# Performance work log

Measured on AMD Instinct MI355X. Metric: run time of the kernel, lower is better.

Reference implementation:

```python
import jax, jax.numpy as jnp
import numpy as np

B, T, D = 64, 32, 256
NFC = 2 * D          # num_inputs_fc = 512
DIMS = [4 * D, NFC, NFC // 2, NFC // 4, NFC // 8, 4]  # last layer padded to 4 outs
H = 4                # camera, rot, trans, plane heads stacked


def setup_inputs() -> dict:
    key = jax.random.key(0)
    ks = jax.random.split(key, 12)
    inp = {
        "emb": jax.random.normal(ks[0], (B, T, D), dtype=jnp.float32),
        # each of n0, n1 in [1,16] so n0+n1 <= T=32 and no divide-by-zero
        "num_planes": jax.random.randint(ks[1], (B, 2), 1, 17, dtype=jnp.int32),
    }
    for i in range(5):
        fan_in = DIMS[i]
        scale = 1.0 / np.sqrt(fan_in)
        inp[f"w{i}"] = jax.random.uniform(ks[2 + 2 * i], (H, DIMS[i], DIMS[i + 1]),
                                           minval=-scale, maxval=scale, dtype=jnp.float32)
        inp[f"b{i}"] = jax.random.uniform(ks[3 + 2 * i], (H, DIMS[i + 1]),
                                           minval=-scale, maxval=scale, dtype=jnp.float32)
    return inp


def _forward(emb, num_planes, w0, b0, w1, b1, w2, b2, w3, b3, w4, b4):
    Bs, Ts, Ds = emb.shape
    n0 = num_planes[:, 0]
    n1 = num_planes[:, 1]
    idx = jnp.arange(Ts)
    # img1 global feature: mean of tokens t < n0 (original zeroes t>=n0 then sums / n0)
    m1 = (idx[None, :] < n0[:, None])                                  # (B,T) bool
    g1 = (emb * m1[..., None].astype(emb.dtype)).sum(1) / n0[:, None].astype(emb.dtype)
    # img2 global feature: mean of tokens n0 <= t < n0+n1
    in2 = (idx[None, :] >= n0[:, None]) & (idx[None, :] < (n0 + n1)[:, None])  # (B,T)
    g2 = (emb * in2[..., None].astype(emb.dtype)).sum(1) / n1[:, None].astype(emb.dtype)
    # pairwise concat: [emb_i, emb_j, g1, g2] -> (B,T,T,4D)
    ei = jnp.broadcast_to(emb[:, :, None, :], (Bs, Ts, Ts, Ds))
    ej = jnp.broadcast_to(emb[:, None, :, :], (Bs, Ts, Ts, Ds))
    g1b = jnp.broadcast_to(g1[:, None, None, :], (Bs, Ts, Ts, Ds))
    g2b = jnp.broadcast_to(g2[:, None, None, :], (Bs, Ts, Ts, Ds))
    cat = jnp.concatenate([ei, ej, g1b, g2b], axis=-1)
    # 4 stacked MLP heads (camera, rot, trans, plane); final layer padded to 4 outputs
    h = jax.nn.relu(jnp.einsum('btsd,hdk->hbtsk', cat, w0) + b0[:, None, None, None, :])
    h = jax.nn.relu(jnp.einsum('hbtsd,hdk->hbtsk', h, w1) + b1[:, None, None, None, :])
    h = jax.nn.relu(jnp.einsum('hbtsd,hdk->hbtsk', h, w2) + b2[:, None, None, None, :])
    h = jax.nn.relu(jnp.einsum('hbtsd,hdk->hbtsk', h, w3) + b3[:, None, None, None, :])
    h = jnp.einsum('hbtsd,hdk->hbtsk', h, w4) + b4[:, None, None, None, :]  # (4,B,T,T,4)
    camera = h[0, ..., 0]            # (B,T,T)
    rot = h[1]                       # (B,T,T,4)
    trans = h[2, ..., :3]            # (B,T,T,3)
    plane_corr = jax.nn.sigmoid(h[3, ..., 0])  # (B,T,T)
    # valid pairs: row i < n0, col j in [n0, n0+n1)  (== ~padding_mask)
    valid = m1[:, :, None] & in2[:, None, :]                           # (B,T,T) bool
    v = valid.astype(emb.dtype)
    pf = (n0 * n1).astype(emb.dtype)
    camera_corr = jax.nn.sigmoid((camera * v).sum((1, 2)) / pf)        # (B,)
    rot_res = (rot * v[..., None]).sum((1, 2)) / pf[:, None]           # (B,4)
    trans_res = (trans * v[..., None]).sum((1, 2)) / pf[:, None]       # (B,3)
    return camera_corr, rot_res, trans_res, plane_corr, valid


def reference(emb, num_planes, w0, b0, w1, b1, w2, b2, w3, b3, w4, b4):
    return _forward(emb, num_planes, w0, b0, w1, b1, w2, b2, w3, b3, w4, b4)
```

## Files before the change

kernel.cpp:

```cpp
#include <hip/hip_runtime.h>

typedef float f32x4 __attribute__((ext_vector_type(4)));
typedef short short8 __attribute__((ext_vector_type(8)));
typedef unsigned short ushort_t;
typedef unsigned int uint_t;

constexpr int O_CAM   = 0;
constexpr int O_ROT   = 64;
constexpr int O_TRANS = 320;
constexpr int O_PLANE = 512;
constexpr int O_VALID = 66048;

constexpr size_t B_G1   = 0;
constexpr size_t B_G2   = 65536;
constexpr size_t B_ACC  = 131072;
constexpr size_t B_ABF  = 133120;
constexpr size_t B_CBF  = 8521728;
constexpr size_t B_BT1  = 16910336;
constexpr size_t B_BT2  = 17958912;
constexpr size_t B_BT3  = 18221056;
constexpr size_t B_BT0F = 18286592;
constexpr size_t B_BT4  = 22480896;

__device__ __forceinline__ ushort_t f2bf(float f) {
    uint_t u = __float_as_uint(f);
    return (ushort_t)((u + 0x7FFFu + ((u >> 16) & 1u)) >> 16);
}

__device__ __forceinline__ uint_t cvt_pk_bf16(float lo, float hi) {
    uint_t r;
    asm("v_cvt_pk_bf16_f32 %0, %1, %2" : "=v"(r) : "v"(lo), "v"(hi));
    return r;
}

__device__ __forceinline__ uint_t bfadd2_relu(uint_t a, uint_t c) {
    const float lo = __uint_as_float(a << 16) + __uint_as_float(c << 16);
    const float hi = __uint_as_float(a & 0xffff0000u) + __uint_as_float(c & 0xffff0000u);
    return cvt_pk_bf16(fmaxf(lo, 0.f), fmaxf(hi, 0.f));
}

__global__ __launch_bounds__(256) void k_prepA(
    const float* __restrict__ emb, const int* __restrict__ np_,
    const float* __restrict__ w0, ushort_t* __restrict__ bt0f,
    float* __restrict__ g1, float* __restrict__ g2)
{
    const int l = threadIdx.x & 63;
    const int c = blockIdx.x * 4 + (threadIdx.x >> 6);
    if (c >= 4160) return;
    if (c < 4096) {
        const int h = c >> 10, ks = (c >> 5) & 31, nt = c & 31;
        const int n = nt*16 + (l & 15);
        const int d0 = ks*32 + ((l >> 4) << 3);
        short8 o;
        #pragma unroll
        for (int j = 0; j < 8; ++j)
            o[j] = (short)f2bf(w0[((size_t)h*1024 + d0 + j)*512 + n]);
        *(short8*)(bt0f + (size_t)c*512 + (size_t)l*8) = o;
    } else {
        const int b = c - 4096;
        const int n0 = np_[2*b], n1 = np_[2*b+1];
        const float* e = emb + (size_t)b*8192;
        #pragma unroll
        for (int dd = 0; dd < 4; ++dd) {
            const int d = l + 64*dd;
            float a1 = 0.f, a2 = 0.f;
            for (int t = 0; t < 32; ++t) {
                float v = e[t*256 + d];
                if (t < n0) a1 += v;
                else if (t < n0 + n1) a2 += v;
            }
            g1[b*256 + d] = a1 / n0;
            g2[b*256 + d] = a2 / n1;
        }
    }
}

__global__ __launch_bounds__(256) void k_ACp(
    const float* __restrict__ emb, const ushort_t* __restrict__ bt0f,
    const float* __restrict__ g1, const float* __restrict__ g2,
    const float* __restrict__ b0,
    ushort_t* __restrict__ Abf, ushort_t* __restrict__ Cbf,
    const float* __restrict__ w1, const float* __restrict__ w2, const float* __restrict__ w3,
    const float* __restrict__ w4,
    ushort_t* __restrict__ bt1, ushort_t* __restrict__ bt2, ushort_t* __restrict__ bt3,
    ushort_t* __restrict__ bt4,
    const int* __restrict__ np_, float* __restrict__ accz, float* __restrict__ out)
{
    const int tid = threadIdx.x;
    const int l = tid & 63;

    if (blockIdx.x >= 512) {
        int c = (blockIdx.x - 512) * 4 + (tid >> 6);
        if (c >= 1417) return;
        if (c < 1344) {
            const float* w; ushort_t* dst; int K, N;
            if (c < 1024)      {           w = w1; dst = bt1 + (size_t)c*512; K = 512; N = 256; }
            else if (c < 1280) { c -= 1024; w = w2; dst = bt2 + (size_t)c*512; K = 256; N = 128; }
            else               { c -= 1280; w = w3; dst = bt3 + (size_t)c*512; K = 128; N = 64;  }
            const int NT = N/16, KS_NT = (K/32)*NT;
            const int h = c / KS_NT, rem = c % KS_NT, ks = rem / NT, nt = rem % NT;
            const int n = nt*16 + (l & 15);
            const int d0 = ks*32 + ((l >> 4) << 3);
            short8 o;
            #pragma unroll
            for (int j = 0; j < 8; ++j)
                o[j] = (short)f2bf(w[((size_t)(h*K + d0 + j))*N + n]);
            *(short8*)(dst + (size_t)l*8) = o;
        } else if (c == 1344) {
            #pragma unroll
            for (int i = 0; i < 8; ++i) accz[l*8 + i] = 0.f;
        } else if (c < 1409) {
            const int b = c - 1345;
            const int n0 = np_[2*b], n1 = np_[2*b+1];
            float* dst = out + O_VALID + b*1024;
            #pragma unroll
            for (int i = 0; i < 16; ++i) {
                const int j = l*16 + i;
                const int t = j >> 5, s = j & 31;
                dst[j] = (t < n0 && s >= n0 && s < n0 + n1) ? 1.f : 0.f;
            }
        } else {
            const int u = c - 1409;
            const int h = u >> 1, ks = u & 1;
            const int n = l & 15;
            const int d0 = ks*32 + ((l >> 4) << 3);
            short8 o;
            #pragma unroll
            for (int j = 0; j < 8; ++j)
                o[j] = (n < 4) ? (short)f2bf(w4[(size_t)h*256 + (d0 + j)*4 + n]) : (short)0;
            *(short8*)(bt4 + ((size_t)u*64 + l)*8) = o;
        }
        return;
    }

    const int b = blockIdx.x & 63, hc = blockIdx.x >> 6;
    const int h = hc >> 1, isC = hc & 1;
    const int w4w = tid >> 6;
    const int lrow = l & 15, lko = l >> 4;

    __shared__ __align__(16) char es[16384];
    __shared__ __align__(16) ushort_t gs[512];

    {
        const float* eb = emb + (size_t)b*8192;
        #pragma unroll
        for (int j = 0; j < 16; ++j) {
            const int flat = j*256 + tid;
            const int row = flat >> 7, cp = flat & 127;
            const float2 v = *(const float2*)(eb + row*256 + cp*2);
            const uint_t p = (uint_t)f2bf(v.x) | ((uint_t)f2bf(v.y) << 16);
            const int byte = (row*512 + cp*4) ^ ((row & 7) << 4);
            *(uint_t*)(es + byte) = p;
        }
    }
    if (!isC && tid < 64) {
        const float* src = (tid < 32) ? (g1 + b*256 + tid*8) : (g2 + b*256 + (tid - 32)*8);
        const float4 v0 = *(const float4*)(src);
        const float4 v1 = *(const float4*)(src + 4);
        short8 o;
        o[0] = (short)f2bf(v0.x); o[1] = (short)f2bf(v0.y);
        o[2] = (short)f2bf(v0.z); o[3] = (short)f2bf(v0.w);
        o[4] = (short)f2bf(v1.x); o[5] = (short)f2bf(v1.y);
        o[6] = (short)f2bf(v1.z); o[7] = (short)f2bf(v1.w);
        *(short8*)(gs + tid*8) = o;
    }
    __syncthreads();

    f32x4 acc[2][8];
    #pragma unroll
    for (int mt = 0; mt < 2; ++mt)
        #pragma unroll
        for (int nt = 0; nt < 8; ++nt) acc[mt][nt] = (f32x4){0.f,0.f,0.f,0.f};

    const ushort_t* basef = bt0f + (size_t)h*(32*32*512) + (size_t)(w4w*8)*512 + (size_t)l*8;

    {
        const int ksE0 = isC ? 8 : 0;
        for (int kk = 0; kk < 8; ++kk) {
            short8 bfv[8];
            const ushort_t* bp = basef + (size_t)(ksE0 + kk)*16384;
            #pragma unroll
            for (int nt = 0; nt < 8; ++nt) bfv[nt] = *(const short8*)(bp + nt*512);
            const int o = (lrow*512 + kk*64 + lko*16) ^ ((lrow & 7) << 4);
            const short8 a0 = *(const short8*)(es + o);
            const short8 a1 = *(const short8*)(es + o + 8192);
            __builtin_amdgcn_s_setprio(1);
            #pragma unroll
            for (int nt = 0; nt < 8; ++nt) {
                acc[0][nt] = __builtin_amdgcn_mfma_f32_16x16x32_bf16(a0, bfv[nt], acc[0][nt], 0, 0, 0);
                acc[1][nt] = __builtin_amdgcn_mfma_f32_16x16x32_bf16(a1, bfv[nt], acc[1][nt], 0, 0, 0);
            }
            __builtin_amdgcn_s_setprio(0);
        }
    }
    if (!isC) {
        for (int kk = 0; kk < 16; ++kk) {
            short8 bfv[8];
            const ushort_t* bp = basef + (size_t)(16 + kk)*16384;
            #pragma unroll
            for (int nt = 0; nt < 8; ++nt) bfv[nt] = *(const short8*)(bp + nt*512);
            const short8 ag = *(const short8*)(gs + kk*32 + lko*8);
            __builtin_amdgcn_s_setprio(1);
            #pragma unroll
            for (int nt = 0; nt < 8; ++nt) {
                acc[0][nt] = __builtin_amdgcn_mfma_f32_16x16x32_bf16(ag, bfv[nt], acc[0][nt], 0, 0, 0);
                acc[1][nt] = __builtin_amdgcn_mfma_f32_16x16x32_bf16(ag, bfv[nt], acc[1][nt], 0, 0, 0);
            }
            __builtin_amdgcn_s_setprio(0);
        }
    }

    ushort_t* dst = (isC ? Cbf : Abf) + (size_t)(h*64 + b)*32*512;
    #pragma unroll
    for (int nt = 0; nt < 8; ++nt) {
        const int col = (w4w*8 + nt)*16 + lrow;
        const float g = isC ? 0.f : b0[h*512 + col];
        #pragma unroll
        for (int mt = 0; mt < 2; ++mt)
            #pragma unroll
            for (int r = 0; r < 4; ++r) {
                const int row = mt*16 + lko*4 + r;
                dst[row*512 + col] = f2bf(acc[mt][nt][r] + g);
            }
    }
}

__global__ __launch_bounds__(512, 2) void k_mlp(
    const ushort_t* __restrict__ Abf, const ushort_t* __restrict__ Cbf,
    const ushort_t* __restrict__ bt1, const ushort_t* __restrict__ bt2,
    const ushort_t* __restrict__ bt3, const ushort_t* __restrict__ bt4,
    const float* __restrict__ b1, const float* __restrict__ b2, const float* __restrict__ b3,
    const float* __restrict__ b4,
    const int* __restrict__ np_, float* __restrict__ out, float* __restrict__ accbuf)
{
    const int x = blockIdx.x;
    const bool isH3 = (x < 1024);
    int h, b, t0;
    int n0 = 0, n1 = 0;
    if (isH3) {
        h = 3; b = x >> 4; t0 = (x & 15) * 2;
    } else {
        const int y = x - 1024;
        h = y >> 8; b = (y >> 2) & 63; t0 = (y & 3) * 4;
        n0 = np_[2*b]; n1 = np_[2*b+1];
        if (t0 >= n0) return;
    }

    __shared__ __align__(16) char smem[65536];
    char* X   = smem;
    char* X2  = smem + 49152;
    char* X3b = smem + 32768;

    const int tid = threadIdx.x;
    const int l = tid & 63, w = tid >> 6;
    const int lrow = l & 15, lko = l >> 4;
    const size_t hb = (size_t)(h*64 + b);
    const uint4* Arows = (const uint4*)(Abf + hb*32*512);
    const uint4* Crows = (const uint4*)(Cbf + hb*32*512);

    const ushort_t* bp1 = bt1 + (size_t)(h*256 + w*2)*512 + (size_t)l*8;
    short8 bb[2][2];
    bb[0][0] = *(const short8*)(bp1);
    bb[0][1] = *(const short8*)(bp1 + 512);

    #pragma unroll
    for (int i = 0; i < 8; ++i) {
        const int flat = i*512 + tid;
        const int row = flat >> 6, q4 = flat & 63;
        int trow, crow;
        if (isH3) { trow = t0 + (row >> 5); crow = row & 31; }
        else      { trow = t0 + (row >> 4); crow = n0 + (row & 15); }
        const uint4 aa = Arows[(size_t)trow*64 + q4];
        const uint4 cc = Crows[(size_t)crow*64 + q4];
        uint4 v;
        v.x = bfadd2_relu(aa.x, cc.x);
        v.y = bfadd2_relu(aa.y, cc.y);
        v.z = bfadd2_relu(aa.z, cc.z);
        v.w = bfadd2_relu(aa.w, cc.w);
        *(uint4*)(X + ((row*1024 + q4*16) ^ ((row & 7) << 4))) = v;
    }
    __syncthreads();

    f32x4 acc1[4][2];
    #pragma unroll
    for (int mt = 0; mt < 4; ++mt)
        #pragma unroll
        for (int nt = 0; nt < 2; ++nt) acc1[mt][nt] = (f32x4){0.f,0.f,0.f,0.f};

    #pragma unroll
    for (int ks = 0; ks < 16; ++ks) {
        if (ks < 15) {
            bb[(ks+1)&1][0] = *(const short8*)(bp1 + (size_t)(ks+1)*8192);
            bb[(ks+1)&1][1] = *(const short8*)(bp1 + (size_t)(ks+1)*8192 + 512);
        }
        const short8 bf0 = bb[ks&1][0];
        const short8 bf1 = bb[ks&1][1];
        __builtin_amdgcn_s_setprio(1);
        #pragma unroll
        for (int mt = 0; mt < 4; ++mt) {
            const short8 a0 = *(const short8*)(X + (((mt*16 + lrow)*1024 + ks*64 + lko*16) ^ ((lrow & 7) << 4)));
            acc1[mt][0] = __builtin_amdgcn_mfma_f32_16x16x32_bf16(a0, bf0, acc1[mt][0], 0, 0, 0);
            acc1[mt][1] = __builtin_amdgcn_mfma_f32_16x16x32_bf16(a0, bf1, acc1[mt][1], 0, 0, 0);
        }
        __builtin_amdgcn_s_setprio(0);
    }
    __syncthreads();

    #pragma unroll
    for (int nt = 0; nt < 2; ++nt) {
        const int col = (w*2 + nt)*16 + lrow;
        const float bias = b1[h*256 + col];
        #pragma unroll
        for (int mt = 0; mt < 4; ++mt)
            #pragma unroll
            for (int r = 0; r < 4; ++r) {
                const int row = mt*16 + lko*4 + r;
                const float v = fmaxf(acc1[mt][nt][r] + bias, 0.f);
                *(ushort_t*)(X + ((row*512 + col*2) ^ ((row & 7) << 4))) =
                    (ushort_t)cvt_pk_bf16(v, v);
            }
    }
    __syncthreads();

    f32x4 acc2[4];
    #pragma unroll
    for (int mt = 0; mt < 4; ++mt) acc2[mt] = (f32x4){0.f,0.f,0.f,0.f};
    {
        const ushort_t* bp = bt2 + (size_t)(h*64 + w)*512 + (size_t)l*8;
        short8 b2b[2];
        b2b[0] = *(const short8*)(bp);
        #pragma unroll
        for (int ks = 0; ks < 8; ++ks) {
            if (ks < 7) b2b[(ks+1)&1] = *(const short8*)(bp + (size_t)(ks+1)*4096);
            __builtin_amdgcn_s_setprio(1);
            #pragma unroll
            for (int mt = 0; mt < 4; ++mt) {
                const short8 a0 = *(const short8*)(X + (((mt*16 + lrow)*512 + ks*64 + lko*16) ^ ((lrow & 7) << 4)));
                acc2[mt] = __builtin_amdgcn_mfma_f32_16x16x32_bf16(a0, b2b[ks&1], acc2[mt], 0, 0, 0);
            }
            __builtin_amdgcn_s_setprio(0);
        }
    }
    {
        const int col = w*16 + lrow;
        const float bias = b2[h*128 + col];
        #pragma unroll
        for (int mt = 0; mt < 4; ++mt)
            #pragma unroll
            for (int r = 0; r < 4; ++r) {
                const int row = mt*16 + lko*4 + r;
                const float v = fmaxf(acc2[mt][r] + bias, 0.f);
                *(ushort_t*)(X2 + ((row*256 + col*2) ^ ((row & 7) << 4))) =
                    (ushort_t)cvt_pk_bf16(v, v);
            }
    }
    __syncthreads();

    const int mhalf = w >> 2;
    f32x4 acc3[2];
    acc3[0] = (f32x4){0.f,0.f,0.f,0.f};
    acc3[1] = (f32x4){0.f,0.f,0.f,0.f};
    {
        const ushort_t* bp = bt3 + (size_t)(h*16 + (w & 3))*512 + (size_t)l*8;
        #pragma unroll
        for (int ks = 0; ks < 4; ++ks) {
            const short8 bf = *(const short8*)(bp + (size_t)ks*2048);
            __builtin_amdgcn_s_setprio(1);
            #pragma unroll
            for (int mi = 0; mi < 2; ++mi) {
                const int mt = mhalf*2 + mi;
                const short8 a0 = *(const short8*)(X2 + (((mt*16 + lrow)*256 + ks*64 + lko*16) ^ ((lrow & 7) << 4)));
                acc3[mi] = __builtin_amdgcn_mfma_f32_16x16x32_bf16(a0, bf, acc3[mi], 0, 0, 0);
            }
            __builtin_amdgcn_s_setprio(0);
        }
    }
    {
        const int col = (w & 3)*16 + lrow;
        const float bias = b3[h*64 + col];
        #pragma unroll
        for (int mi = 0; mi < 2; ++mi) {
            const int mt = mhalf*2 + mi;
            #pragma unroll
            for (int r = 0; r < 4; ++r) {
                const int row = mt*16 + lko*4 + r;
                const float v = fmaxf(acc3[mi][r] + bias, 0.f);
                *(ushort_t*)(X3b + ((row*128 + col*2) ^ ((row & 7) << 4))) =
                    (ushort_t)cvt_pk_bf16(v, v);
            }
        }
    }
    __syncthreads();

    if (w < 4) {
        const int mt = w;
        f32x4 acc4 = (f32x4){0.f,0.f,0.f,0.f};
        const ushort_t* bp = bt4 + (size_t)(h*2)*512 + (size_t)l*8;
        #pragma unroll
        for (int ks = 0; ks < 2; ++ks) {
            const short8 bf = *(const short8*)(bp + (size_t)ks*512);
            const short8 a0 = *(const short8*)(X3b + (((mt*16 + lrow)*128 + ks*64 + lko*16) ^ ((lrow & 7) << 4)));
            acc4 = __builtin_amdgcn_mfma_f32_16x16x32_bf16(a0, bf, acc4, 0, 0, 0);
        }
        const float bias = b4[h*4 + (lrow & 3)];
        #pragma unroll
        for (int r = 0; r < 4; ++r) acc4[r] += bias;

        if (isH3) {
            if (lrow == 0) {
                #pragma unroll
                for (int r = 0; r < 4; ++r) {
                    const int row = mt*16 + lko*4 + r;
                    out[O_PLANE + b*1024 + (t0 + (row >> 5))*32 + (row & 31)] =
                        1.f / (1.f + expf(-acc4[r]));
                }
            }
        } else {
            const int nj = (h == 0) ? 1 : ((h == 1) ? 4 : 3);
            float v = 0.f;
            #pragma unroll
            for (int r = 0; r < 4; ++r) {
                const int row = mt*16 + lko*4 + r;
                const int tq = row >> 4, sr = row & 15;
                if ((t0 + tq) < n0 && sr < n1) v += acc4[r];
            }
            v += __shfl_down(v, 32);
            v += __shfl_down(v, 16);
            if (lko == 0 && lrow < nj) {
                const int slot = (h == 0) ? 0 : ((h == 1) ? 1 + lrow : 5 + lrow);
                atomicAdd(&accbuf[b*8 + slot], v);
            }
        }
    }
}

__global__ __launch_bounds__(512) void k_final(
    const int* __restrict__ np_, const float* __restrict__ acc, float* __restrict__ out)
{
    const int tid = threadIdx.x;
    const int b = tid >> 3, sl = tid & 7;
    const int n0 = np_[2*b], n1 = np_[2*b+1];
    const float pf = (float)(n0 * n1);
    const float v = acc[b*8 + sl] / pf;
    if (sl == 0)      out[O_CAM + b] = 1.f / (1.f + expf(-v));
    else if (sl <= 4) out[O_ROT + b*4 + (sl - 1)] = v;
    else              out[O_TRANS + b*3 + (sl - 5)] = v;
}

extern "C" void kernel_launch(void* const* d_in, const int* in_sizes, int n_in,
                              void* d_out, int out_size, void* d_ws, size_t ws_size,
                              hipStream_t stream) {
    (void)in_sizes; (void)n_in; (void)out_size; (void)ws_size;
    const float* emb = (const float*)d_in[0];
    const int*   np_ = (const int*)d_in[1];
    const float* w0  = (const float*)d_in[2];
    const float* b0  = (const float*)d_in[3];
    const float* w1  = (const float*)d_in[4];
    const float* b1  = (const float*)d_in[5];
    const float* w2  = (const float*)d_in[6];
    const float* b2  = (const float*)d_in[7];
    const float* w3  = (const float*)d_in[8];
    const float* b3  = (const float*)d_in[9];
    const float* w4  = (const float*)d_in[10];
    const float* b4  = (const float*)d_in[11];

    char* W = (char*)d_ws;
    float* out = (float*)d_out;
    float*    g1   = (float*)(W + B_G1);
    float*    g2   = (float*)(W + B_G2);
    float*    acc  = (float*)(W + B_ACC);
    ushort_t* Abf  = (ushort_t*)(W + B_ABF);
    ushort_t* Cbf  = (ushort_t*)(W + B_CBF);
    ushort_t* bt1  = (ushort_t*)(W + B_BT1);
    ushort_t* bt2  = (ushort_t*)(W + B_BT2);
    ushort_t* bt3  = (ushort_t*)(W + B_BT3);
    ushort_t* bt0f = (ushort_t*)(W + B_BT0F);
    ushort_t* bt4  = (ushort_t*)(W + B_BT4);

    k_prepA<<<1040, 256, 0, stream>>>(emb, np_, w0, bt0f, g1, g2);
    k_ACp<<<867, 256, 0, stream>>>(emb, bt0f, g1, g2, b0, Abf, Cbf,
                                   w1, w2, w3, w4, bt1, bt2, bt3, bt4, np_, acc, out);
    k_mlp<<<1792, 512, 0, stream>>>(Abf, Cbf, bt1, bt2, bt3, bt4,
                                    b1, b2, b3, b4, np_, out, acc);
    k_final<<<1, 512, 0, stream>>>(np_, acc, out);
}
```

Baseline: 85.25 us.

## Keep layer-0 partial products in fp32 and stage weight transposes through LDS

The per-token layer-0 partial products A and C are now stored as fp32 instead of bf16, so the add-and-ReLU in the MLP kernel happens on full-precision values before a single bf16 rounding. Weight prepack kernels now read w0..w3 with coalesced float4 loads into a shared-memory staging tile and then transpose from LDS, replacing strided scalar global reads. The fp32 intermediates double the bytes written by k_ACp and read by k_mlp. The gain is in accuracy and prepack coalescing, paid for with extra memory traffic. The staging relies on an lgkmcnt wait with no barrier, which is valid only because each wave reads just its own slice of the tile.

```diff
diff --git a/kernel.cpp b/kernel.cpp
--- a/kernel.cpp
+++ b/kernel.cpp
@@ -14,13 +14,13 @@
 constexpr size_t B_G1   = 0;
 constexpr size_t B_G2   = 65536;
 constexpr size_t B_ACC  = 131072;
-constexpr size_t B_ABF  = 133120;
-constexpr size_t B_CBF  = 8521728;
-constexpr size_t B_BT1  = 16910336;
-constexpr size_t B_BT2  = 17958912;
-constexpr size_t B_BT3  = 18221056;
-constexpr size_t B_BT0F = 18286592;
-constexpr size_t B_BT4  = 22480896;
+constexpr size_t B_AF   = 133120;
+constexpr size_t B_CF   = 16910336;
+constexpr size_t B_BT1  = 33687552;
+constexpr size_t B_BT2  = 34736128;
+constexpr size_t B_BT3  = 34998272;
+constexpr size_t B_BT0F = 35063808;
+constexpr size_t B_BT4  = 39258112;
 
 __device__ __forceinline__ ushort_t f2bf(float f) {
     uint_t u = __float_as_uint(f);
@@ -31,12 +31,6 @@
     uint_t r;
     asm("v_cvt_pk_bf16_f32 %0, %1, %2" : "=v"(r) : "v"(lo), "v"(hi));
     return r;
-}
-
-__device__ __forceinline__ uint_t bfadd2_relu(uint_t a, uint_t c) {
-    const float lo = __uint_as_float(a << 16) + __uint_as_float(c << 16);
-    const float hi = __uint_as_float(a & 0xffff0000u) + __uint_as_float(c & 0xffff0000u);
-    return cvt_pk_bf16(fmaxf(lo, 0.f), fmaxf(hi, 0.f));
 }
 
 __global__ __launch_bounds__(256) void k_prepA(
@@ -44,17 +38,24 @@
     const float* __restrict__ w0, ushort_t* __restrict__ bt0f,
     float* __restrict__ g1, float* __restrict__ g2)
 {
+    __shared__ float stg[4][32][18];
     const int l = threadIdx.x & 63;
-    const int c = blockIdx.x * 4 + (threadIdx.x >> 6);
+    const int u = threadIdx.x >> 6;
+    const int c = blockIdx.x * 4 + u;
     if (c >= 4160) return;
     if (c < 4096) {
         const int h = c >> 10, ks = (c >> 5) & 31, nt = c & 31;
-        const int n = nt*16 + (l & 15);
-        const int d0 = ks*32 + ((l >> 4) << 3);
+        const float* src = w0 + ((size_t)h*1024 + ks*32 + (l >> 1))*512 + nt*16 + (l & 1)*8;
+        const float4 v0 = *(const float4*)(src);
+        const float4 v1 = *(const float4*)(src + 4);
+        float* srow = &stg[u][l >> 1][(l & 1)*8];
+        srow[0]=v0.x; srow[1]=v0.y; srow[2]=v0.z; srow[3]=v0.w;
+        srow[4]=v1.x; srow[5]=v1.y; srow[6]=v1.z; srow[7]=v1.w;
+        asm volatile("s_waitcnt lgkmcnt(0)" ::: "memory");
+        const int d0 = (l >> 4) << 3, n = l & 15;
         short8 o;
         #pragma unroll
-        for (int j = 0; j < 8; ++j)
-            o[j] = (short)f2bf(w0[((size_t)h*1024 + d0 + j)*512 + n]);
+        for (int j = 0; j < 8; ++j) o[j] = (short)f2bf(stg[u][d0 + j][n]);
         *(short8*)(bt0f + (size_t)c*512 + (size_t)l*8) = o;
     } else {
         const int b = c - 4096;
@@ -79,18 +80,23 @@
     const float* __restrict__ emb, const ushort_t* __restrict__ bt0f,
     const float* __restrict__ g1, const float* __restrict__ g2,
     const float* __restrict__ b0,
-    ushort_t* __restrict__ Abf, ushort_t* __restrict__ Cbf,
+    float* __restrict__ Af, float* __restrict__ Cf,
     const float* __restrict__ w1, const float* __restrict__ w2, const float* __restrict__ w3,
     const float* __restrict__ w4,
     ushort_t* __restrict__ bt1, ushort_t* __restrict__ bt2, ushort_t* __restrict__ bt3,
     ushort_t* __restrict__ bt4,
     const int* __restrict__ np_, float* __restrict__ accz, float* __restrict__ out)
 {
+    __shared__ __align__(16) char es[16384];
+    __shared__ __align__(16) ushort_t gs[512];
+    __shared__ float stg[4][32][18];
+
     const int tid = threadIdx.x;
     const int l = tid & 63;
 
     if (blockIdx.x >= 512) {
-        int c = (blockIdx.x - 512) * 4 + (tid >> 6);
+        const int u = tid >> 6;
+        int c = (blockIdx.x - 512) * 4 + u;
         if (c >= 1417) return;
         if (c < 1344) {
             const float* w; ushort_t* dst; int K, N;
@@ -99,12 +105,17 @@
             else               { c -= 1280; w = w3; dst = bt3 + (size_t)c*512; K = 128; N = 64;  }
             const int NT = N/16, KS_NT = (K/32)*NT;
             const int h = c / KS_NT, rem = c % KS_NT, ks = rem / NT, nt = rem % NT;
-            const int n = nt*16 + (l & 15);
-            const int d0 = ks*32 + ((l >> 4) << 3);
+            const float* src = w + ((size_t)h*K + ks*32 + (l >> 1))*N + nt*16 + (l & 1)*8;
+            const float4 v0 = *(const float4*)(src);
+            const float4 v1 = *(const float4*)(src + 4);
+            float* srow = &stg[u][l >> 1][(l & 1)*8];
+            srow[0]=v0.x; srow[1]=v0.y; srow[2]=v0.z; srow[3]=v0.w;
+            srow[4]=v1.x; srow[5]=v1.y; srow[6]=v1.z; srow[7]=v1.w;
+            asm volatile("s_waitcnt lgkmcnt(0)" ::: "memory");
+            const int d0 = (l >> 4) << 3, n = l & 15;
             short8 o;
             #pragma unroll
-            for (int j = 0; j < 8; ++j)
-                o[j] = (short)f2bf(w[((size_t)(h*K + d0 + j))*N + n]);
+            for (int j = 0; j < 8; ++j) o[j] = (short)f2bf(stg[u][d0 + j][n]);
             *(short8*)(dst + (size_t)l*8) = o;
         } else if (c == 1344) {
             #pragma unroll
@@ -120,15 +131,15 @@
                 dst[j] = (t < n0 && s >= n0 && s < n0 + n1) ? 1.f : 0.f;
             }
         } else {
-            const int u = c - 1409;
-            const int h = u >> 1, ks = u & 1;
+            const int uu = c - 1409;
+            const int h = uu >> 1, ks = uu & 1;
             const int n = l & 15;
             const int d0 = ks*32 + ((l >> 4) << 3);
             short8 o;
             #pragma unroll
             for (int j = 0; j < 8; ++j)
                 o[j] = (n < 4) ? (short)f2bf(w4[(size_t)h*256 + (d0 + j)*4 + n]) : (short)0;
-            *(short8*)(bt4 + ((size_t)u*64 + l)*8) = o;
+            *(short8*)(bt4 + ((size_t)uu*64 + l)*8) = o;
         }
         return;
     }
@@ -137,9 +148,6 @@
     const int h = hc >> 1, isC = hc & 1;
     const int w4w = tid >> 6;
     const int lrow = l & 15, lko = l >> 4;
-
-    __shared__ __align__(16) char es[16384];
-    __shared__ __align__(16) ushort_t gs[512];
 
     {
         const float* eb = emb + (size_t)b*8192;
@@ -210,7 +218,7 @@
         }
     }
 
-    ushort_t* dst = (isC ? Cbf : Abf) + (size_t)(h*64 + b)*32*512;
+    float* dst = (isC ? Cf : Af) + (size_t)(h*64 + b)*32*512;
     #pragma unroll
     for (int nt = 0; nt < 8; ++nt) {
         const int col = (w4w*8 + nt)*16 + lrow;
@@ -220,13 +228,13 @@
             #pragma unroll
             for (int r = 0; r < 4; ++r) {
                 const int row = mt*16 + lko*4 + r;
-                dst[row*512 + col] = f2bf(acc[mt][nt][r] + g);
+                dst[row*512 + col] = acc[mt][nt][r] + g;
             }
     }
 }
 
 __global__ __launch_bounds__(512, 2) void k_mlp(
-    const ushort_t* __restrict__ Abf, const ushort_t* __restrict__ Cbf,
+    const float* __restrict__ Af, const float* __restrict__ Cf,
     const ushort_t* __restrict__ bt1, const ushort_t* __restrict__ bt2,
     const ushort_t* __restrict__ bt3, const ushort_t* __restrict__ bt4,
     const float* __restrict__ b1, const float* __restrict__ b2, const float* __restrict__ b3,
@@ -255,8 +263,8 @@
     const int l = tid & 63, w = tid >> 6;
     const int lrow = l & 15, lko = l >> 4;
     const size_t hb = (size_t)(h*64 + b);
-    const uint4* Arows = (const uint4*)(Abf + hb*32*512);
-    const uint4* Crows = (const uint4*)(Cbf + hb*32*512);
+    const float4* ArF = (const float4*)(Af + hb*32*512);
+    const float4* CrF = (const float4*)(Cf + hb*32*512);
 
     const ushort_t* bp1 = bt1 + (size_t)(h*256 + w*2)*512 + (size_t)l*8;
     short8 bb[2][2];
@@ -270,13 +278,15 @@
         int trow, crow;
         if (isH3) { trow = t0 + (row >> 5); crow = row & 31; }
         else      { trow = t0 + (row >> 4); crow = n0 + (row & 15); }
-        const uint4 aa = Arows[(size_t)trow*64 + q4];
-        const uint4 cc = Crows[(size_t)crow*64 + q4];
+        const float4 a0 = ArF[(size_t)trow*128 + q4*2];
+        const float4 a1 = ArF[(size_t)trow*128 + q4*2 + 1];
+        const float4 c0 = CrF[(size_t)crow*128 + q4*2];
+        const float4 c1 = CrF[(size_t)crow*128 + q4*2 + 1];
         uint4 v;
-        v.x = bfadd2_relu(aa.x, cc.x);
-        v.y = bfadd2_relu(aa.y, cc.y);
-        v.z = bfadd2_relu(aa.z, cc.z);
-        v.w = bfadd2_relu(aa.w, cc.w);
+        v.x = cvt_pk_bf16(fmaxf(a0.x + c0.x, 0.f), fmaxf(a0.y + c0.y, 0.f));
+        v.y = cvt_pk_bf16(fmaxf(a0.z + c0.z, 0.f), fmaxf(a0.w + c0.w, 0.f));
+        v.z = cvt_pk_bf16(fmaxf(a1.x + c1.x, 0.f), fmaxf(a1.y + c1.y, 0.f));
+        v.w = cvt_pk_bf16(fmaxf(a1.z + c1.z, 0.f), fmaxf(a1.w + c1.w, 0.f));
         *(uint4*)(X + ((row*1024 + q4*16) ^ ((row & 7) << 4))) = v;
     }
     __syncthreads();
@@ -469,8 +479,8 @@
     float*    g1   = (float*)(W + B_G1);
     float*    g2   = (float*)(W + B_G2);
     float*    acc  = (float*)(W + B_ACC);
-    ushort_t* Abf  = (ushort_t*)(W + B_ABF);
-    ushort_t* Cbf  = (ushort_t*)(W + B_CBF);
+    float*    Af   = (float*)(W + B_AF);
+    float*    Cf   = (float*)(W + B_CF);
     ushort_t* bt1  = (ushort_t*)(W + B_BT1);
     ushort_t* bt2  = (ushort_t*)(W + B_BT2);
     ushort_t* bt3  = (ushort_t*)(W + B_BT3);
@@ -478,9 +488,9 @@
     ushort_t* bt4  = (ushort_t*)(W + B_BT4);
 
     k_prepA<<<1040, 256, 0, stream>>>(emb, np_, w0, bt0f, g1, g2);
-    k_ACp<<<867, 256, 0, stream>>>(emb, bt0f, g1, g2, b0, Abf, Cbf,
+    k_ACp<<<867, 256, 0, stream>>>(emb, bt0f, g1, g2, b0, Af, Cf,
                                    w1, w2, w3, w4, bt1, bt2, bt3, bt4, np_, acc, out);
-    k_mlp<<<1792, 512, 0, stream>>>(Abf, Cbf, bt1, bt2, bt3, bt4,
+    k_mlp<<<1792, 512, 0, stream>>>(Af, Cf, bt1, bt2, bt3, bt4,
                                     b1, b2, b3, b4, np_, out, acc);
     k_final<<<1, 512, 0, stream>>>(np_, acc, out);
 }
```

Result: slower. 90.38 us (+6.0%).
